# Kernel optimization log

Hardware: AMD Instinct MI355X
Metric: run time of the kernel (lower is better)

## Reference

```python
import jax, jax.numpy as jnp
import numpy as np

NUM_SITES = 64
PHYS_DIM = 2
BOND_DIM = 32
BATCH = 65536


def _build_mps(num_sites, phys_dim, bond_dim, seed=0):
    """Replicates ImprovedMPS._initialize_tensors + _canonical_form, then
    zero-pads ragged cores into a dense [S, D, p, D] stack."""
    rng = np.random.default_rng(seed)
    tensors = []
    cur = 1
    for i in range(num_sites):
        if i == 0:
            nb = min(bond_dim, phys_dim)
            shape = (1, phys_dim, nb)
            cur = nb
        elif i == num_sites - 1:
            shape = (cur, phys_dim, 1)
        else:
            nb = min(bond_dim, cur * phys_dim)
            shape = (cur, phys_dim, nb)
            cur = nb
        ld, rd = shape[0] * shape[1], shape[2]
        m = (rng.standard_normal((ld, rd)) * 0.1).astype(np.float32)
        if ld >= rd:
            q, _ = np.linalg.qr(m)
            t = q.reshape(shape)
        else:
            q, _ = np.linalg.qr(m.T)
            t = q.T.reshape(shape)
        tensors.append(t.astype(np.float32))
    # left-canonical sweep
    for i in range(num_sites - 1):
        l, p, r = tensors[i].shape
        q, rr = np.linalg.qr(tensors[i].reshape(l * p, r))
        tensors[i] = q.reshape(l, p, q.shape[1]).astype(np.float32)
        nl, npd, nr = tensors[i + 1].shape
        tensors[i + 1] = (rr @ tensors[i + 1].reshape(nl, npd * nr)).reshape(rr.shape[0], npd, nr).astype(np.float32)
    # zero-pad ragged bonds into dense stack [S, D, p, D]
    A = np.zeros((num_sites, bond_dim, phys_dim, bond_dim), dtype=np.float32)
    for i, t in enumerate(tensors):
        l, p, r = t.shape
        A[i, :l, :, :r] = t
    return A


def setup_inputs() -> dict:
    key = jax.random.key(0)
    x_batch = jax.random.normal(key, (BATCH, NUM_SITES, PHYS_DIM), dtype=jnp.float32)
    A = jnp.asarray(_build_mps(NUM_SITES, PHYS_DIM, BOND_DIM))
    return {"x_batch": x_batch, "A": A}


def reference(x_batch, A):
    # x_batch: [B, S, p]; A: [S, D, p, D] (zero-padded ragged MPS cores)
    B = x_batch.shape[0]
    D = A.shape[1]
    # left_vector starts as ones(B,1) in the ragged view == one-hot e0 in padded view
    left0 = jnp.zeros((B, D), dtype=x_batch.dtype).at[:, 0].set(1.0)
    xs = jnp.moveaxis(x_batch, 1, 0)  # [S, B, p]

    def step(left, inp):
        A_i, x_i = inp  # [D, p, D], [B, p]
        # fuses: contracted = einsum('bp,lpd->bld'); left = einsum('bl,bld->bd')
        left = jnp.einsum('bl,bp,lpd->bd', left, x_i, A_i)
        return left, None

    left, _ = jax.lax.scan(step, left0, (A, xs))
    return left[:, :1]  # last core has right bond 1 -> only col 0 is nonzero
```

## Files before the change

### kernel.cpp

```cpp
#include <hip/hip_runtime.h>


typedef _Float16 half8 __attribute__((ext_vector_type(8)));
typedef _Float16 half4 __attribute__((ext_vector_type(4)));
typedef float floatx16 __attribute__((ext_vector_type(16)));
typedef float f32x4 __attribute__((ext_vector_type(4)));

#define NPAIRS 32
#define GCH 8192
#define XSTRIDE 129

__global__ void mps_prep_pair(const float* __restrict__ A, _Float16* __restrict__ Gf) {
    __shared__ float sA[1024];
    __shared__ float sB[1024];
    __shared__ float sG[1024];
    const int blk = blockIdx.x;
    const int P   = blk >> 2;
    const int pq  = blk & 3;
    const int p   = pq >> 1, q = pq & 1;
    const int tid = threadIdx.x;
    const int row = tid >> 3;
    const int c4  = (tid & 7) * 4;

    *(f32x4*)&sA[row * 32 + c4] =
        *(const f32x4*)(A + ((size_t)(2 * P) * 32 + row) * 64 + p * 32 + c4);
    *(f32x4*)&sB[row * 32 + c4] =
        *(const f32x4*)(A + ((size_t)(2 * P + 1) * 32 + row) * 64 + q * 32 + c4);
    __syncthreads();

    {
        f32x4 acc;
        acc[0] = 0.f; acc[1] = 0.f; acc[2] = 0.f; acc[3] = 0.f;
        for (int m = 0; m < 32; ++m) {
            const float av = sA[row * 32 + m];
            const f32x4 bv = *(const f32x4*)&sB[m * 32 + c4];
            acc[0] += av * bv[0]; acc[1] += av * bv[1];
            acc[2] += av * bv[2]; acc[3] += av * bv[3];
        }
        *(f32x4*)&sG[row * 32 + c4] = acc;
    }
    __syncthreads();

    if (tid < 128) {
        const int lh   = tid >> 6;
        const int lane = tid & 63;
        const int h    = lane >> 5;
        const int d    = lane & 31;
        half8 v;
#pragma unroll
        for (int e = 0; e < 8; ++e) {
            const int l = 16 * lh + (e & 3) + 8 * (e >> 2) + 4 * h;
            v[e] = (_Float16)sG[l * 32 + d];
        }
        reinterpret_cast<half8*>(Gf)[((size_t)P * 8 + pq * 2 + lh) * 64 + lane] = v;
    }
}

#define MF32(A_, B_, C_) __builtin_amdgcn_mfma_f32_32x32x16_f16(A_, B_, C_, 0, 0, 0)

#define STAGEG(C, BUF)                                                        \
    {                                                                         \
        _Pragma("unroll")                                                     \
        for (int r_ = 0; r_ < 4; ++r_) {                                      \
            const int rec_ = r_ * 4 + wid;                                    \
            const _Float16* g_ = Gf + (size_t)(C) * GCH + rec_ * 512 + lane * 8; \
            __builtin_amdgcn_global_load_lds(                                 \
                (const __attribute__((address_space(1))) void*)g_,            \
                (__attribute__((address_space(3))) void*)&smG[(BUF) * GCH + rec_ * 512], \
                16, 0, 0);                                                    \
        }                                                                     \
    }

#define PAIRDO(BUF, LP, P)                                                    \
    {                                                                         \
        const half4 xq_ = smX[(P) * XSTRIDE + r];                             \
        const _Float16 w00_ = xq_[0] * xq_[2];                                \
        const _Float16 w01_ = xq_[0] * xq_[3];                                \
        const _Float16 w10_ = xq_[1] * xq_[2];                                \
        const _Float16 w11_ = xq_[1] * xq_[3];                                \
        half8 G_[8];                                                          \
        _Pragma("unroll")                                                     \
        for (int f_ = 0; f_ < 8; ++f_)                                        \
            G_[f_] = *(const half8*)&smG[(BUF) * GCH + (((LP) * 8 + f_) * 64 + lane) * 8]; \
        half8 FA0_, FA1_;                                                     \
        _Pragma("unroll")                                                     \
        for (int i_ = 0; i_ < 8; ++i_) {                                      \
            FA0_[i_] = (_Float16)acc[i_];                                     \
            FA1_[i_] = (_Float16)acc[8 + i_];                                 \
        }                                                                     \
        floatx16 t_;                                                          \
        t_ = MF32(G_[0], FA0_ * w00_, zv);                                    \
        t_ = MF32(G_[1], FA1_ * w00_, t_);                                    \
        t_ = MF32(G_[2], FA0_ * w01_, t_);                                    \
        t_ = MF32(G_[3], FA1_ * w01_, t_);                                    \
        t_ = MF32(G_[4], FA0_ * w10_, t_);                                    \
        t_ = MF32(G_[5], FA1_ * w10_, t_);                                    \
        t_ = MF32(G_[6], FA0_ * w11_, t_);                                    \
        t_ = MF32(G_[7], FA1_ * w11_, t_);                                    \
        acc = t_;                                                             \
    }

#define CHUNK(C, BUF)                                                         \
    {                                                                         \
        if ((C) < 15) STAGEG((C) + 1, 1 - (BUF));                             \
        PAIRDO(BUF, 0, 2 * (C))                                               \
        PAIRDO(BUF, 1, 2 * (C) + 1)                                           \
        __syncthreads();                                                      \
    }

__global__ __launch_bounds__(256, 2) void mps_main(const float* __restrict__ x,
                                                   const _Float16* __restrict__ Gf,
                                                   float* __restrict__ out) {
    __shared__ __align__(16) _Float16 smG[2 * GCH];
    __shared__ __align__(8)  half4    smX[32 * XSTRIDE];

    const int tid  = threadIdx.x;
    const int lane = tid & 63;
    const int wid  = tid >> 6;
    const int brow = blockIdx.x * 128;
    const int col  = lane & 31;
    const int r    = wid * 32 + col;

    STAGEG(0, 0);

#pragma unroll
    for (int i = 0; i < 16; ++i) {
        const int j   = i * 256 + tid;
        const int row = j >> 5, q = j & 31;
        const f32x4 v = *(const f32x4*)(x + (size_t)(brow + row) * 128 + 4 * q);
        half4 hv;
        hv[0] = (_Float16)v[0]; hv[1] = (_Float16)v[1];
        hv[2] = (_Float16)v[2]; hv[3] = (_Float16)v[3];
        smX[q * XSTRIDE + row] = hv;
    }

    floatx16 zv;
#pragma unroll
    for (int i = 0; i < 16; ++i) zv[i] = 0.f;

    floatx16 acc;
#pragma unroll
    for (int i = 0; i < 16; ++i) acc[i] = 0.f;
    if (lane < 32) acc[0] = 1.f;

    __syncthreads();

    CHUNK(0, 0)   CHUNK(1, 1)   CHUNK(2, 0)   CHUNK(3, 1)
    CHUNK(4, 0)   CHUNK(5, 1)   CHUNK(6, 0)   CHUNK(7, 1)
    CHUNK(8, 0)   CHUNK(9, 1)   CHUNK(10, 0)  CHUNK(11, 1)
    CHUNK(12, 0)  CHUNK(13, 1)  CHUNK(14, 0)  CHUNK(15, 1)

    if (lane < 32) out[brow + wid * 32 + lane] = acc[0];
}

extern "C" void kernel_launch(void* const* d_in, const int* in_sizes, int n_in,
                              void* d_out, int out_size, void* d_ws, size_t ws_size,
                              hipStream_t stream) {
    const float* x = (const float*)d_in[0];
    const float* A = (const float*)d_in[1];
    float* outp = (float*)d_out;
    _Float16* Gf = (_Float16*)d_ws;

    hipLaunchKernelGGL(mps_prep_pair, dim3(NPAIRS * 4), dim3(256), 0, stream, A, Gf);
    hipLaunchKernelGGL(mps_main, dim3(65536 / 128), dim3(256), 0, stream, x, Gf, outp);
}
```

Measured before the change: 30.16 us.

## Triple-buffer per-pair G stages with vmcnt-based barriers and precompute x weights

Restructures the G staging from double-buffered 2-pair chunks (8192 halves) into a 3-deep ring of single-pair stages (4096 halves), prefetching two stages ahead. Uses explicit s_waitcnt vmcnt(2) plus s_barrier in place of a full __syncthreads, so the most recent loads can remain in flight. The outer-product x weights (x0*x2 etc.) are now computed once in fp32 during the x staging instead of in fp16 per pair. LDS use drops from 2x8192 to 3x4096 halves, and correctness now depends on the hand-written wait counts.

```diff
diff --git a/kernel.cpp b/kernel.cpp
--- a/kernel.cpp
+++ b/kernel.cpp
@@ -7,7 +7,7 @@
 typedef float f32x4 __attribute__((ext_vector_type(4)));
 
 #define NPAIRS 32
-#define GCH 8192
+#define GCH1 4096
 #define XSTRIDE 129
 
 __global__ void mps_prep_pair(const float* __restrict__ A, _Float16* __restrict__ Gf) {
@@ -27,7 +27,6 @@
     *(f32x4*)&sB[row * 32 + c4] =
         *(const f32x4*)(A + ((size_t)(2 * P + 1) * 32 + row) * 64 + q * 32 + c4);
     __syncthreads();
-
     {
         f32x4 acc;
         acc[0] = 0.f; acc[1] = 0.f; acc[2] = 0.f; acc[3] = 0.f;
@@ -40,7 +39,6 @@
         *(f32x4*)&sG[row * 32 + c4] = acc;
     }
     __syncthreads();
-
     if (tid < 128) {
         const int lh   = tid >> 6;
         const int lane = tid & 63;
@@ -58,30 +56,29 @@
 
 #define MF32(A_, B_, C_) __builtin_amdgcn_mfma_f32_32x32x16_f16(A_, B_, C_, 0, 0, 0)
 
-#define STAGEG(C, BUF)                                                        \
+#define PB2() asm volatile("s_waitcnt vmcnt(2)\n\ts_barrier" ::: "memory")
+#define PB0() asm volatile("s_waitcnt vmcnt(0)\n\ts_barrier" ::: "memory")
+
+#define STAGE1(C, BUF)                                                        \
     {                                                                         \
         _Pragma("unroll")                                                     \
-        for (int r_ = 0; r_ < 4; ++r_) {                                      \
+        for (int r_ = 0; r_ < 2; ++r_) {                                      \
             const int rec_ = r_ * 4 + wid;                                    \
-            const _Float16* g_ = Gf + (size_t)(C) * GCH + rec_ * 512 + lane * 8; \
+            const _Float16* g_ = Gf + (size_t)(C) * GCH1 + rec_ * 512 + lane * 8; \
             __builtin_amdgcn_global_load_lds(                                 \
                 (const __attribute__((address_space(1))) void*)g_,            \
-                (__attribute__((address_space(3))) void*)&smG[(BUF) * GCH + rec_ * 512], \
+                (__attribute__((address_space(3))) void*)&smG[(BUF) * GCH1 + rec_ * 512], \
                 16, 0, 0);                                                    \
         }                                                                     \
     }
 
-#define PAIRDO(BUF, LP, P)                                                    \
+#define PAIRDO(BUF, P)                                                        \
     {                                                                         \
-        const half4 xq_ = smX[(P) * XSTRIDE + r];                             \
-        const _Float16 w00_ = xq_[0] * xq_[2];                                \
-        const _Float16 w01_ = xq_[0] * xq_[3];                                \
-        const _Float16 w10_ = xq_[1] * xq_[2];                                \
-        const _Float16 w11_ = xq_[1] * xq_[3];                                \
+        const half4 xw_ = smX[(P) * XSTRIDE + r];                             \
         half8 G_[8];                                                          \
         _Pragma("unroll")                                                     \
         for (int f_ = 0; f_ < 8; ++f_)                                        \
-            G_[f_] = *(const half8*)&smG[(BUF) * GCH + (((LP) * 8 + f_) * 64 + lane) * 8]; \
+            G_[f_] = *(const half8*)&smG[(BUF) * GCH1 + ((f_ * 64 + lane)) * 8]; \
         half8 FA0_, FA1_;                                                     \
         _Pragma("unroll")                                                     \
         for (int i_ = 0; i_ < 8; ++i_) {                                      \
@@ -89,29 +86,21 @@
             FA1_[i_] = (_Float16)acc[8 + i_];                                 \
         }                                                                     \
         floatx16 t_;                                                          \
-        t_ = MF32(G_[0], FA0_ * w00_, zv);                                    \
-        t_ = MF32(G_[1], FA1_ * w00_, t_);                                    \
-        t_ = MF32(G_[2], FA0_ * w01_, t_);                                    \
-        t_ = MF32(G_[3], FA1_ * w01_, t_);                                    \
-        t_ = MF32(G_[4], FA0_ * w10_, t_);                                    \
-        t_ = MF32(G_[5], FA1_ * w10_, t_);                                    \
-        t_ = MF32(G_[6], FA0_ * w11_, t_);                                    \
-        t_ = MF32(G_[7], FA1_ * w11_, t_);                                    \
+        t_ = MF32(G_[0], FA0_ * xw_[0], zv);                                  \
+        t_ = MF32(G_[1], FA1_ * xw_[0], t_);                                  \
+        t_ = MF32(G_[2], FA0_ * xw_[1], t_);                                  \
+        t_ = MF32(G_[3], FA1_ * xw_[1], t_);                                  \
+        t_ = MF32(G_[4], FA0_ * xw_[2], t_);                                  \
+        t_ = MF32(G_[5], FA1_ * xw_[2], t_);                                  \
+        t_ = MF32(G_[6], FA0_ * xw_[3], t_);                                  \
+        t_ = MF32(G_[7], FA1_ * xw_[3], t_);                                  \
         acc = t_;                                                             \
-    }
-
-#define CHUNK(C, BUF)                                                         \
-    {                                                                         \
-        if ((C) < 15) STAGEG((C) + 1, 1 - (BUF));                             \
-        PAIRDO(BUF, 0, 2 * (C))                                               \
-        PAIRDO(BUF, 1, 2 * (C) + 1)                                           \
-        __syncthreads();                                                      \
     }
 
 __global__ __launch_bounds__(256, 2) void mps_main(const float* __restrict__ x,
                                                    const _Float16* __restrict__ Gf,
                                                    float* __restrict__ out) {
-    __shared__ __align__(16) _Float16 smG[2 * GCH];
+    __shared__ __align__(16) _Float16 smG[3 * GCH1];
     __shared__ __align__(8)  half4    smX[32 * XSTRIDE];
 
     const int tid  = threadIdx.x;
@@ -121,7 +110,8 @@
     const int col  = lane & 31;
     const int r    = wid * 32 + col;
 
-    STAGEG(0, 0);
+    STAGE1(0, 0);
+    STAGE1(1, 1);
 
 #pragma unroll
     for (int i = 0; i < 16; ++i) {
@@ -129,8 +119,8 @@
         const int row = j >> 5, q = j & 31;
         const f32x4 v = *(const f32x4*)(x + (size_t)(brow + row) * 128 + 4 * q);
         half4 hv;
-        hv[0] = (_Float16)v[0]; hv[1] = (_Float16)v[1];
-        hv[2] = (_Float16)v[2]; hv[3] = (_Float16)v[3];
+        hv[0] = (_Float16)(v[0] * v[2]); hv[1] = (_Float16)(v[0] * v[3]);
+        hv[2] = (_Float16)(v[1] * v[2]); hv[3] = (_Float16)(v[1] * v[3]);
         smX[q * XSTRIDE + row] = hv;
     }
 
@@ -145,10 +135,13 @@
 
     __syncthreads();
 
-    CHUNK(0, 0)   CHUNK(1, 1)   CHUNK(2, 0)   CHUNK(3, 1)
-    CHUNK(4, 0)   CHUNK(5, 1)   CHUNK(6, 0)   CHUNK(7, 1)
-    CHUNK(8, 0)   CHUNK(9, 1)   CHUNK(10, 0)  CHUNK(11, 1)
-    CHUNK(12, 0)  CHUNK(13, 1)  CHUNK(14, 0)  CHUNK(15, 1)
+#pragma unroll
+    for (int C = 0; C < 32; ++C) {
+        if (C < 30) STAGE1(C + 2, (C + 2) % 3);
+        PAIRDO(C % 3, C)
+        if (C < 30)      PB2();
+        else if (C == 30) PB0();
+    }
 
     if (lane < 32) out[brow + wid * 32 + lane] = acc[0];
 }
```

Result: no change. 30.59 us (+1.4%).

## Read pair cores directly from global memory instead of staging via LDS

Applied to the files above, without the earlier changes.

Drops the double-buffered global-to-LDS staging of the fused pair cores and the per-chunk block barriers. Each wave now loads its MFMA A-operand fragments straight from global memory (L2/L1-cached, shared by all blocks) inside a fully unrolled 32-pair loop. This removes LDS traffic and __syncthreads, and frees 32KB of LDS per block. The cost is that global-load latency now sits directly on the serial MFMA dependency chain, relying on the compiler to hoist loads ahead.

```diff
diff --git a/kernel.cpp b/kernel.cpp
--- a/kernel.cpp
+++ b/kernel.cpp
@@ -7,7 +7,6 @@
 typedef float f32x4 __attribute__((ext_vector_type(4)));
 
 #define NPAIRS 32
-#define GCH 8192
 #define XSTRIDE 129
 
 __global__ void mps_prep_pair(const float* __restrict__ A, _Float16* __restrict__ Gf) {
@@ -27,7 +26,6 @@
     *(f32x4*)&sB[row * 32 + c4] =
         *(const f32x4*)(A + ((size_t)(2 * P + 1) * 32 + row) * 64 + q * 32 + c4);
     __syncthreads();
-
     {
         f32x4 acc;
         acc[0] = 0.f; acc[1] = 0.f; acc[2] = 0.f; acc[3] = 0.f;
@@ -40,7 +38,6 @@
         *(f32x4*)&sG[row * 32 + c4] = acc;
     }
     __syncthreads();
-
     if (tid < 128) {
         const int lh   = tid >> 6;
         const int lane = tid & 63;
@@ -58,20 +55,7 @@
 
 #define MF32(A_, B_, C_) __builtin_amdgcn_mfma_f32_32x32x16_f16(A_, B_, C_, 0, 0, 0)
 
-#define STAGEG(C, BUF)                                                        \
-    {                                                                         \
-        _Pragma("unroll")                                                     \
-        for (int r_ = 0; r_ < 4; ++r_) {                                      \
-            const int rec_ = r_ * 4 + wid;                                    \
-            const _Float16* g_ = Gf + (size_t)(C) * GCH + rec_ * 512 + lane * 8; \
-            __builtin_amdgcn_global_load_lds(                                 \
-                (const __attribute__((address_space(1))) void*)g_,            \
-                (__attribute__((address_space(3))) void*)&smG[(BUF) * GCH + rec_ * 512], \
-                16, 0, 0);                                                    \
-        }                                                                     \
-    }
-
-#define PAIRDO(BUF, LP, P)                                                    \
+#define PAIRDO(P)                                                             \
     {                                                                         \
         const half4 xq_ = smX[(P) * XSTRIDE + r];                             \
         const _Float16 w00_ = xq_[0] * xq_[2];                                \
@@ -81,7 +65,7 @@
         half8 G_[8];                                                          \
         _Pragma("unroll")                                                     \
         for (int f_ = 0; f_ < 8; ++f_)                                        \
-            G_[f_] = *(const half8*)&smG[(BUF) * GCH + (((LP) * 8 + f_) * 64 + lane) * 8]; \
+            G_[f_] = gfp[((P) * 8 + f_) * 64 + lane];                         \
         half8 FA0_, FA1_;                                                     \
         _Pragma("unroll")                                                     \
         for (int i_ = 0; i_ < 8; ++i_) {                                      \
@@ -100,19 +84,10 @@
         acc = t_;                                                             \
     }
 
-#define CHUNK(C, BUF)                                                         \
-    {                                                                         \
-        if ((C) < 15) STAGEG((C) + 1, 1 - (BUF));                             \
-        PAIRDO(BUF, 0, 2 * (C))                                               \
-        PAIRDO(BUF, 1, 2 * (C) + 1)                                           \
-        __syncthreads();                                                      \
-    }
-
 __global__ __launch_bounds__(256, 2) void mps_main(const float* __restrict__ x,
                                                    const _Float16* __restrict__ Gf,
                                                    float* __restrict__ out) {
-    __shared__ __align__(16) _Float16 smG[2 * GCH];
-    __shared__ __align__(8)  half4    smX[32 * XSTRIDE];
+    __shared__ __align__(8) half4 smX[32 * XSTRIDE];
 
     const int tid  = threadIdx.x;
     const int lane = tid & 63;
@@ -121,7 +96,7 @@
     const int col  = lane & 31;
     const int r    = wid * 32 + col;
 
-    STAGEG(0, 0);
+    const half8* gfp = reinterpret_cast<const half8*>(Gf);
 
 #pragma unroll
     for (int i = 0; i < 16; ++i) {
@@ -145,10 +120,10 @@
 
     __syncthreads();
 
-    CHUNK(0, 0)   CHUNK(1, 1)   CHUNK(2, 0)   CHUNK(3, 1)
-    CHUNK(4, 0)   CHUNK(5, 1)   CHUNK(6, 0)   CHUNK(7, 1)
-    CHUNK(8, 0)   CHUNK(9, 1)   CHUNK(10, 0)  CHUNK(11, 1)
-    CHUNK(12, 0)  CHUNK(13, 1)  CHUNK(14, 0)  CHUNK(15, 1)
+#pragma unroll
+    for (int P = 0; P < 32; ++P) {
+        PAIRDO(P)
+    }
 
     if (lane < 32) out[brow + wid * 32 + lane] = acc[0];
 }
```

Measured after the change: 38.64 us. +28.1%, slower.
